# Performance work log

Hardware: AMD Instinct MI355X
Metric: run time of the kernel (lower is better)

The kernel has to match this reference:

```python
import jax, jax.numpy as jnp
import numpy as np

B, S, D = 32, 2048, 8
H = 256
COUPLING = -1.0  # TC['WOBBLE_COUPLING'] default
WOBBLE_STEP = 0.03125


def setup_inputs() -> dict:
    key = jax.random.key(0)
    k = jax.random.split(key, 5)
    return {
        'x': jax.random.normal(k[0], (B, S, D), dtype=jnp.float32),
        'We': jax.random.normal(k[1], (H, D), dtype=jnp.float32) * 0.35,
        'be': jax.random.normal(k[2], (H,), dtype=jnp.float32) * 0.02,
        'Wr': jax.random.normal(k[3], (256, 7 * H), dtype=jnp.float32) * 0.02,
        'br': jax.random.normal(k[4], (256,), dtype=jnp.float32) * 0.02,
    }


def _forward(x, We, be, Wr, br):
    Bm, Sm, _ = x.shape
    h = We.shape[0]

    def step(carry, xt):
        ph, wb, prev_xt, has_prev = carry
        pt = xt @ We.T + be                      # [B,h] embedded phase increments
        # xpt = stack([cos(pt), sin(pt)]); accumulator consumes the spinor pair,
        # equivalent to the wrapped phase delta atan2(sin, cos)
        delta = jnp.arctan2(jnp.sin(pt), jnp.cos(pt))
        wb2 = wb + WOBBLE_STEP
        is_rep = has_prev * jnp.all(xt == prev_xt, axis=1, keepdims=True).astype(x.dtype)
        # WobblePhaseAccumulator(spinor=True): phase advances by delta plus
        # coupling-modulated wobble; wobble channel accumulates delta
        ph_out = ph + delta + COUPLING * jnp.sin(wb2)
        wb_out = wb2 + delta
        ph_new = ph_out
        wb_new = is_rep * wb_out + (1.0 - is_rep) * wb2
        ph_s = 0.5 * ph_new
        readout = jnp.concatenate([
            jnp.cos(ph_new), jnp.sin(ph_new),
            jnp.cos(ph_s), jnp.sin(ph_s),
            jnp.cos(wb_new), jnp.sin(wb_new),
            ph_new,
        ], axis=1)                                # [B, 7h]
        logits = readout @ Wr.T + br              # [B, 256]
        return (ph_new, wb_new, xt, jnp.ones((), x.dtype)), (logits, ph_new, wb_new)

    ph0 = jnp.zeros((Bm, h), x.dtype)
    wb0 = jnp.zeros((Bm, h), x.dtype)
    prev0 = jnp.zeros((Bm, x.shape[2]), x.dtype)
    carry0 = (ph0, wb0, prev0, jnp.zeros((), x.dtype))
    xs = jnp.swapaxes(x, 0, 1)                    # [S,B,D]
    _, (logits, ph_hist, wb_hist) = jax.lax.scan(step, carry0, xs)
    logits = jnp.swapaxes(logits, 0, 1)           # [B,S,256]
    ph_hist = jnp.swapaxes(ph_hist, 0, 1)         # [B,S,h]
    wb_hist = jnp.swapaxes(wb_hist, 0, 1)         # [B,S,h]
    return logits, ph_hist, wb_hist


def reference(x, We, be, Wr, br):
    return _forward(x, We, be, Wr, br)
```

## Files before the change

### kernel.cpp

```cpp
#include <hip/hip_runtime.h>
#include <hip/hip_bf16.h>
#include <math.h>

#define NB 32
#define NS 2048
#define ND 8
#define NH 256
#define NK 1792
#define NO 256
#define NM (NB*NS)
#define WSTEP 0.03125f
#define CCH 64
#define LCH (NS/CCH)

typedef __attribute__((ext_vector_type(8))) short short8;
typedef __attribute__((ext_vector_type(4))) float f32x4;

__device__ float g_ssum[NB*CCH*NH];
__device__ float g_wb0 [NB*CCH*NH];
__device__ float g_esum[NB*CCH*NH];
__device__ float g_ph0 [NB*CCH*NH];
__device__ float g_rep [NB*NS];
__device__ unsigned short g_bb[NO*NK];

__device__ __forceinline__ unsigned short bf16_rn(float f){
    union { float f; unsigned int u; } v; v.f = f;
    unsigned int u = v.u;
    unsigned int r = (u + 0x7FFFu + ((u >> 16) & 1u)) >> 16;
    return (unsigned short)r;
}

extern "C" __global__ __launch_bounds__(256)
void k_delta(const float* __restrict__ x, const float* __restrict__ We,
             const float* __restrict__ be, float* __restrict__ delta){
    int blk = blockIdx.x;
    int b = blk >> 6;
    int c = blk & (CCH-1);
    int t0 = c * LCH;
    int h = threadIdx.x;
    __shared__ float xs[(LCH+1)*ND];
    __shared__ float rep[LCH];

    for(int i = h; i < (LCH+1)*ND/4; i += 256){
        int row  = i >> 1;
        int col4 = (i & 1) * 4;
        int t = t0 - 1 + row; if(t < 0) t = 0;
        *(float4*)&xs[row*ND + col4] = *(const float4*)&x[((size_t)b*NS + t)*ND + col4];
    }
    __syncthreads();
    if(h < LCH){
        int t = t0 + h;
        float fl = 0.f;
        if(t > 0){
            bool eq = true;
            #pragma unroll
            for(int d2 = 0; d2 < ND; ++d2) eq = eq && (xs[(h+1)*ND+d2] == xs[h*ND+d2]);
            fl = eq ? 1.f : 0.f;
        }
        rep[h] = fl;
        g_rep[b*NS + t] = fl;
    }
    __syncthreads();

    float4 w0 = *(const float4*)&We[h*ND];
    float4 w1 = *(const float4*)&We[h*ND + 4];
    float bh = be[h];
    float ssum = 0.f;
    for(int j = 0; j < LCH; ++j){
        const float* xr = &xs[(j+1)*ND];
        float pt = bh + xr[0]*w0.x + xr[1]*w0.y + xr[2]*w0.z + xr[3]*w0.w
                      + xr[4]*w1.x + xr[5]*w1.y + xr[6]*w1.z + xr[7]*w1.w;
        float s, cc;
        sincosf(pt, &s, &cc);
        float d = atan2f(s, cc);
        delta[((size_t)(t0+j)*NB + b)*NH + h] = d;
        ssum += WSTEP + rep[j]*d;
    }
    g_ssum[(b*CCH + c)*NH + h] = ssum;
}

extern "C" __global__ __launch_bounds__(256)
void k_prefix_s(){
    int g = blockIdx.x*256 + threadIdx.x;
    int b = g >> 8, h = g & 255;
    float acc = 0.f;
    for(int c = 0; c < CCH; ++c){
        size_t idx = ((size_t)(b*CCH + c))*NH + h;
        g_wb0[idx] = acc;
        acc += g_ssum[idx];
    }
}
extern "C" __global__ __launch_bounds__(256)
void k_prefix_e(){
    int g = blockIdx.x*256 + threadIdx.x;
    int b = g >> 8, h = g & 255;
    float acc = 0.f;
    for(int c = 0; c < CCH; ++c){
        size_t idx = ((size_t)(b*CCH + c))*NH + h;
        g_ph0[idx] = acc;
        acc += g_esum[idx];
    }
}

extern "C" __global__ __launch_bounds__(256)
void k_escan(const float* __restrict__ delta, float* __restrict__ wb_hist){
    int blk = blockIdx.x;
    int b = blk >> 6, c = blk & (CCH-1), t0 = c*LCH, h = threadIdx.x;
    __shared__ float rep[LCH];
    if(h < LCH) rep[h] = g_rep[b*NS + t0 + h];
    __syncthreads();
    float wb = g_wb0[(b*CCH + c)*NH + h];
    const float* dp = delta + (size_t)t0*NB*NH + b*NH + h;
    float* wp = wb_hist + ((size_t)b*NS + t0)*NH + h;
    float d[LCH];
    #pragma unroll
    for(int j = 0; j < LCH; ++j) d[j] = dp[(size_t)j*(NB*NH)];
    float esum = 0.f;
    #pragma unroll
    for(int j = 0; j < LCH; ++j){
        float wb2 = wb + WSTEP;
        float e = d[j] - sinf(wb2);
        esum += e;
        wb = wb2 + rep[j]*d[j];
        wp[(size_t)j*NH] = wb;
    }
    g_esum[(b*CCH + c)*NH + h] = esum;
}

extern "C" __global__ __launch_bounds__(256)
void k_phw(const float* __restrict__ delta, float* __restrict__ ph_hist){
    int blk = blockIdx.x;
    int b = blk >> 6, c = blk & (CCH-1), t0 = c*LCH, h = threadIdx.x;
    __shared__ float rep[LCH];
    if(h < LCH) rep[h] = g_rep[b*NS + t0 + h];
    __syncthreads();
    float wb = g_wb0[(b*CCH + c)*NH + h];
    float ph = g_ph0[(b*CCH + c)*NH + h];
    const float* dp = delta + (size_t)t0*NB*NH + b*NH + h;
    float* pp = ph_hist + ((size_t)b*NS + t0)*NH + h;
    float d[LCH];
    #pragma unroll
    for(int j = 0; j < LCH; ++j) d[j] = dp[(size_t)j*(NB*NH)];
    #pragma unroll
    for(int j = 0; j < LCH; ++j){
        float wb2 = wb + WSTEP;
        float e = d[j] - sinf(wb2);
        ph += e;
        wb = wb2 + rep[j]*d[j];
        pp[(size_t)j*NH] = ph;
    }
}

extern "C" __global__ __launch_bounds__(256)
void k_bconv(const float* __restrict__ Wr){
    int i = (blockIdx.x*256 + threadIdx.x) * 8;
    if(i >= NO*NK) return;
    float4 a = *(const float4*)&Wr[i];
    float4 b = *(const float4*)&Wr[i+4];
    union { unsigned int u[4]; uint4 v; } r;
    r.u[0] = (unsigned int)bf16_rn(a.x) | ((unsigned int)bf16_rn(a.y) << 16);
    r.u[1] = (unsigned int)bf16_rn(a.z) | ((unsigned int)bf16_rn(a.w) << 16);
    r.u[2] = (unsigned int)bf16_rn(b.x) | ((unsigned int)bf16_rn(b.y) << 16);
    r.u[3] = (unsigned int)bf16_rn(b.z) | ((unsigned int)bf16_rn(b.w) << 16);
    *(uint4*)&g_bb[i] = r.v;
}

#define DO_CH(CH, SRC) do{                                                        \
    short8 bfr[4];                                                                \
    _Pragma("unroll")                                                             \
    for(int nf = 0; nf < 4; ++nf)                                                 \
        bfr[nf] = *(const short8*)&g_bb[(size_t)(colb + nf*16)*NK + (CH)*256 + hb];\
    short8 afr[4];                                                                \
    _Pragma("unroll")                                                             \
    for(int mf = 0; mf < 4; ++mf){                                                \
        union{ unsigned int u[4]; short8 s; } r_;                                 \
        _Pragma("unroll")                                                         \
        for(int j = 0; j < 4; ++j)                                                \
            r_.u[j] = (unsigned int)bf16_rn(SRC[mf][2*j])                         \
                    | ((unsigned int)bf16_rn(SRC[mf][2*j+1]) << 16);              \
        afr[mf] = r_.s;                                                           \
    }                                                                             \
    _Pragma("unroll")                                                             \
    for(int mf = 0; mf < 4; ++mf)                                                 \
        _Pragma("unroll")                                                         \
        for(int nf = 0; nf < 4; ++nf)                                             \
            acc[mf][nf] = __builtin_amdgcn_mfma_f32_16x16x32_bf16(                \
                afr[mf], bfr[nf], acc[mf][nf], 0, 0, 0);                          \
}while(0)

extern "C" __global__ __launch_bounds__(512, 2)
void k_logits(const float* __restrict__ ph_hist, const float* __restrict__ wb_hist,
              const float* __restrict__ br, float* __restrict__ logits){
    int tid  = threadIdx.x;
    int m0   = blockIdx.x * 128;
    int lane = tid & 63, wid = tid >> 6;
    int wm = wid >> 2, wn = wid & 3;
    int l15 = lane & 15, kg = lane >> 4;
    int row0 = m0 + wm*64 + l15;
    int colb = wn*64 + l15;

    f32x4 acc[4][4];
    f32x4 zz = {0.f, 0.f, 0.f, 0.f};
    #pragma unroll
    for(int i = 0; i < 4; ++i)
        #pragma unroll
        for(int j = 0; j < 4; ++j) acc[i][j] = zz;

    for(int hc = 0; hc < 8; ++hc){
        int hb = hc*32 + kg*8;
        float a0[4][8], s8[4][8], c8[4][8];

        #pragma unroll
        for(int mf = 0; mf < 4; ++mf){
            const float* p = ph_hist + (size_t)(row0 + mf*16)*NH + hb;
            float4 x0 = *(const float4*)p;
            float4 x1 = *(const float4*)(p + 4);
            a0[mf][0]=x0.x; a0[mf][1]=x0.y; a0[mf][2]=x0.z; a0[mf][3]=x0.w;
            a0[mf][4]=x1.x; a0[mf][5]=x1.y; a0[mf][6]=x1.z; a0[mf][7]=x1.w;
        }
        DO_CH(6, a0);

        #pragma unroll
        for(int mf = 0; mf < 4; ++mf)
            #pragma unroll
            for(int j = 0; j < 8; ++j){
                float r = a0[mf][j] * 0.07957747154594767f;
                r -= floorf(r);
                s8[mf][j] = __builtin_amdgcn_sinf(r);
                c8[mf][j] = __builtin_amdgcn_cosf(r);
            }
        DO_CH(2, c8);
        DO_CH(3, s8);

        #pragma unroll
        for(int mf = 0; mf < 4; ++mf)
            #pragma unroll
            for(int j = 0; j < 8; ++j)
                a0[mf][j] = c8[mf][j]*c8[mf][j] - s8[mf][j]*s8[mf][j];
        DO_CH(0, a0);
        #pragma unroll
        for(int mf = 0; mf < 4; ++mf)
            #pragma unroll
            for(int j = 0; j < 8; ++j)
                a0[mf][j] = 2.f * s8[mf][j] * c8[mf][j];
        DO_CH(1, a0);

        #pragma unroll
        for(int mf = 0; mf < 4; ++mf){
            const float* p = wb_hist + (size_t)(row0 + mf*16)*NH + hb;
            float4 x0 = *(const float4*)p;
            float4 x1 = *(const float4*)(p + 4);
            a0[mf][0]=x0.x; a0[mf][1]=x0.y; a0[mf][2]=x0.z; a0[mf][3]=x0.w;
            a0[mf][4]=x1.x; a0[mf][5]=x1.y; a0[mf][6]=x1.z; a0[mf][7]=x1.w;
        }
        #pragma unroll
        for(int mf = 0; mf < 4; ++mf)
            #pragma unroll
            for(int j = 0; j < 8; ++j){
                float r = a0[mf][j] * 0.15915494309189535f;
                r -= floorf(r);
                s8[mf][j] = __builtin_amdgcn_sinf(r);
                c8[mf][j] = __builtin_amdgcn_cosf(r);
            }
        DO_CH(4, c8);
        DO_CH(5, s8);
    }

    int lg = kg;
    #pragma unroll
    for(int nf = 0; nf < 4; ++nf){
        int col = wn*64 + nf*16 + l15;
        float bias = br[col];
        #pragma unroll
        for(int mf = 0; mf < 4; ++mf){
            int row = m0 + wm*64 + mf*16 + lg*4;
            #pragma unroll
            for(int r = 0; r < 4; ++r)
                logits[(size_t)(row + r)*NO + col] = acc[mf][nf][r] + bias;
        }
    }
}

extern "C" void kernel_launch(void* const* d_in, const int* in_sizes, int n_in,
                              void* d_out, int out_size, void* d_ws, size_t ws_size,
                              hipStream_t stream){
    const float* x  = (const float*)d_in[0];
    const float* We = (const float*)d_in[1];
    const float* be = (const float*)d_in[2];
    const float* Wr = (const float*)d_in[3];
    const float* br = (const float*)d_in[4];

    float* logits = (float*)d_out;
    float* ph     = logits + (size_t)NM*NO;
    float* wb     = ph + (size_t)NM*NH;
    float* delta  = logits;

    hipLaunchKernelGGL(k_bconv,    dim3((NO*NK/8 + 255)/256), dim3(256), 0, stream, Wr);
    hipLaunchKernelGGL(k_delta,    dim3(NB*CCH), dim3(256), 0, stream, x, We, be, delta);
    hipLaunchKernelGGL(k_prefix_s, dim3(32),     dim3(256), 0, stream);
    hipLaunchKernelGGL(k_escan,    dim3(NB*CCH), dim3(256), 0, stream, delta, wb);
    hipLaunchKernelGGL(k_prefix_e, dim3(32),     dim3(256), 0, stream);
    hipLaunchKernelGGL(k_phw,      dim3(NB*CCH), dim3(256), 0, stream, delta, ph);
    hipLaunchKernelGGL(k_logits,   dim3(NM/128), dim3(512), 0, stream, ph, wb, br, logits);
}
```

Measured before the change: 447.1 us.

## Stage bf16 readout tile in LDS so each thread computes features once

In the old logits kernel, every wave redundantly loaded ph/wb rows and computed the sin/cos features for its 64-row slice. The four column waves sharing a row block all repeated this. Now all 512 threads cooperatively compute one 128x32 bf16 A tile per k-step, write it to shared memory, and each wave reads its MFMA fragments from LDS. This removes the 4x redundant transcendental work and global loads, and drops the double-angle trick in favour of direct sin/cos per channel. In exchange it adds two __syncthreads per k-step across 56 steps, uses a packed bf16 convert instruction, and raises the occupancy hint to 4 blocks.

Result: faster. 415.4 us (-7.1%).

```diff
diff --git a/kernel.cpp b/kernel.cpp
--- a/kernel.cpp
+++ b/kernel.cpp
@@ -165,39 +165,17 @@
     *(uint4*)&g_bb[i] = r.v;
 }
 
-#define DO_CH(CH, SRC) do{                                                        \
-    short8 bfr[4];                                                                \
-    _Pragma("unroll")                                                             \
-    for(int nf = 0; nf < 4; ++nf)                                                 \
-        bfr[nf] = *(const short8*)&g_bb[(size_t)(colb + nf*16)*NK + (CH)*256 + hb];\
-    short8 afr[4];                                                                \
-    _Pragma("unroll")                                                             \
-    for(int mf = 0; mf < 4; ++mf){                                                \
-        union{ unsigned int u[4]; short8 s; } r_;                                 \
-        _Pragma("unroll")                                                         \
-        for(int j = 0; j < 4; ++j)                                                \
-            r_.u[j] = (unsigned int)bf16_rn(SRC[mf][2*j])                         \
-                    | ((unsigned int)bf16_rn(SRC[mf][2*j+1]) << 16);              \
-        afr[mf] = r_.s;                                                           \
-    }                                                                             \
-    _Pragma("unroll")                                                             \
-    for(int mf = 0; mf < 4; ++mf)                                                 \
-        _Pragma("unroll")                                                         \
-        for(int nf = 0; nf < 4; ++nf)                                             \
-            acc[mf][nf] = __builtin_amdgcn_mfma_f32_16x16x32_bf16(                \
-                afr[mf], bfr[nf], acc[mf][nf], 0, 0, 0);                          \
-}while(0)
-
-extern "C" __global__ __launch_bounds__(512, 2)
+extern "C" __global__ __launch_bounds__(512, 4)
 void k_logits(const float* __restrict__ ph_hist, const float* __restrict__ wb_hist,
               const float* __restrict__ br, float* __restrict__ logits){
+    __shared__ __align__(16) unsigned short Al[128][40];
     int tid  = threadIdx.x;
     int m0   = blockIdx.x * 128;
     int lane = tid & 63, wid = tid >> 6;
     int wm = wid >> 2, wn = wid & 3;
     int l15 = lane & 15, kg = lane >> 4;
-    int row0 = m0 + wm*64 + l15;
     int colb = wn*64 + l15;
+    int arow = tid >> 2, ah = (tid & 3) * 8;
 
     f32x4 acc[4][4];
     f32x4 zz = {0.f, 0.f, 0.f, 0.f};
@@ -206,74 +184,60 @@
         #pragma unroll
         for(int j = 0; j < 4; ++j) acc[i][j] = zz;
 
-    for(int hc = 0; hc < 8; ++hc){
-        int hb = hc*32 + kg*8;
-        float a0[4][8], s8[4][8], c8[4][8];
-
-        #pragma unroll
-        for(int mf = 0; mf < 4; ++mf){
-            const float* p = ph_hist + (size_t)(row0 + mf*16)*NH + hb;
-            float4 x0 = *(const float4*)p;
-            float4 x1 = *(const float4*)(p + 4);
-            a0[mf][0]=x0.x; a0[mf][1]=x0.y; a0[mf][2]=x0.z; a0[mf][3]=x0.w;
-            a0[mf][4]=x1.x; a0[mf][5]=x1.y; a0[mf][6]=x1.z; a0[mf][7]=x1.w;
+    for(int ks = 0; ks < 56; ++ks){
+        int c    = ks >> 3;
+        int kcol = (ks & 7) * 32;
+
+        const float* src = (c == 4 || c == 5) ? wb_hist : ph_hist;
+        const float* p = src + (size_t)(m0 + arow)*NH + kcol + ah;
+        float4 x0 = *(const float4*)p;
+        float4 x1 = *(const float4*)(p + 4);
+        float v[8] = {x0.x, x0.y, x0.z, x0.w, x1.x, x1.y, x1.z, x1.w};
+        if(c != 6){
+            float sc = (c == 2 || c == 3) ? 0.07957747154594767f
+                                          : 0.15915494309189535f;
+            bool is_sin = (c & 1);
+            #pragma unroll
+            for(int j = 0; j < 8; ++j){
+                float r = v[j] * sc;
+                r -= floorf(r);
+                v[j] = is_sin ? __builtin_amdgcn_sinf(r) : __builtin_amdgcn_cosf(r);
+            }
         }
-        DO_CH(6, a0);
-
+        union { unsigned int u[4]; uint4 q; } pk;
+        #pragma unroll
+        for(int j = 0; j < 4; ++j)
+            asm("v_cvt_pk_bf16_f32 %0, %1, %2"
+                : "=v"(pk.u[j]) : "v"(v[2*j]), "v"(v[2*j+1]));
+
+        short8 bfr[4];
+        #pragma unroll
+        for(int nf = 0; nf < 4; ++nf)
+            bfr[nf] = *(const short8*)&g_bb[(size_t)(colb + nf*16)*NK + c*256 + kcol + kg*8];
+
+        __syncthreads();
+        *(uint4*)&Al[arow][ah] = pk.q;
+        __syncthreads();
+
+        short8 afr[4];
         #pragma unroll
         for(int mf = 0; mf < 4; ++mf)
-            #pragma unroll
-            for(int j = 0; j < 8; ++j){
-                float r = a0[mf][j] * 0.07957747154594767f;
-                r -= floorf(r);
-                s8[mf][j] = __builtin_amdgcn_sinf(r);
-                c8[mf][j] = __builtin_amdgcn_cosf(r);
-            }
-        DO_CH(2, c8);
-        DO_CH(3, s8);
-
+            afr[mf] = *(const short8*)&Al[wm*64 + mf*16 + l15][kg*8];
         #pragma unroll
         for(int mf = 0; mf < 4; ++mf)
             #pragma unroll
-            for(int j = 0; j < 8; ++j)
-                a0[mf][j] = c8[mf][j]*c8[mf][j] - s8[mf][j]*s8[mf][j];
-        DO_CH(0, a0);
-        #pragma unroll
-        for(int mf = 0; mf < 4; ++mf)
-            #pragma unroll
-            for(int j = 0; j < 8; ++j)
-                a0[mf][j] = 2.f * s8[mf][j] * c8[mf][j];
-        DO_CH(1, a0);
-
-        #pragma unroll
-        for(int mf = 0; mf < 4; ++mf){
-            const float* p = wb_hist + (size_t)(row0 + mf*16)*NH + hb;
-            float4 x0 = *(const float4*)p;
-            float4 x1 = *(const float4*)(p + 4);
-            a0[mf][0]=x0.x; a0[mf][1]=x0.y; a0[mf][2]=x0.z; a0[mf][3]=x0.w;
-            a0[mf][4]=x1.x; a0[mf][5]=x1.y; a0[mf][6]=x1.z; a0[mf][7]=x1.w;
-        }
-        #pragma unroll
-        for(int mf = 0; mf < 4; ++mf)
-            #pragma unroll
-            for(int j = 0; j < 8; ++j){
-                float r = a0[mf][j] * 0.15915494309189535f;
-                r -= floorf(r);
-                s8[mf][j] = __builtin_amdgcn_sinf(r);
-                c8[mf][j] = __builtin_amdgcn_cosf(r);
-            }
-        DO_CH(4, c8);
-        DO_CH(5, s8);
-    }
-
-    int lg = kg;
+            for(int nf = 0; nf < 4; ++nf)
+                acc[mf][nf] = __builtin_amdgcn_mfma_f32_16x16x32_bf16(
+                    afr[mf], bfr[nf], acc[mf][nf], 0, 0, 0);
+    }
+
     #pragma unroll
     for(int nf = 0; nf < 4; ++nf){
         int col = wn*64 + nf*16 + l15;
         float bias = br[col];
         #pragma unroll
         for(int mf = 0; mf < 4; ++mf){
-            int row = m0 + wm*64 + mf*16 + lg*4;
+            int row = m0 + wm*64 + mf*16 + kg*4;
             #pragma unroll
             for(int r = 0; r < 4; ++r)
                 logits[(size_t)(row + r)*NO + col] = acc[mf][nf][r] + bias;
```
